# Kernel tuning notes

Measured on AMD Instinct MI355X. Metric: run time of the kernel, lower is better.

## Reference

```python
import jax, jax.numpy as jnp
import numpy as np

B, T, HID = 2, 2048, 3840
H, KV, D = 16, 8, 256
EPS = 1e-6
WINDOW = 1024
THETA_LOCAL = 10000.0
THETA_GLOBAL = 1000000.0


def _rope_tables(theta, t, d):
    inv_freq = 1.0 / (theta ** (jnp.arange(0, d, 2, dtype=jnp.float32) / d))  # (d/2,)
    ang = jnp.arange(t, dtype=jnp.float32)[:, None] * inv_freq[None, :]        # (T, d/2)
    return jnp.cos(ang), jnp.sin(ang)


def setup_inputs() -> dict:
    key = jax.random.key(0)
    ks = jax.random.split(key, 8)
    x = jax.random.normal(ks[0], (B, T, HID), dtype=jnp.float32)
    wq = jax.random.normal(ks[1], (H * D, HID), dtype=jnp.float32) * 0.02
    wk = jax.random.normal(ks[2], (KV * D, HID), dtype=jnp.float32) * 0.02
    wv = jax.random.normal(ks[3], (KV * D, HID), dtype=jnp.float32) * 0.02
    wo = jax.random.normal(ks[4], (HID, H * D), dtype=jnp.float32) * 0.02
    q_norm_w = 1.0 + jax.random.normal(ks[5], (D,), dtype=jnp.float32) * 0.02
    k_norm_w = 1.0 + jax.random.normal(ks[6], (D,), dtype=jnp.float32) * 0.02
    cos_g, sin_g = _rope_tables(THETA_GLOBAL, T, D)
    cos_l, sin_l = _rope_tables(THETA_LOCAL, T, D)
    # causal + sliding-window(1024) additive float mask, shape (1,1,T,T)
    i = jnp.arange(T)[:, None]
    j = jnp.arange(T)[None, :]
    allowed = (j <= i) & (i - j < WINDOW)
    attention_mask = jnp.where(allowed, 0.0, -1e9).astype(jnp.float32)[None, None]
    return {"x": x, "cos_global": cos_g, "sin_global": sin_g, "cos_local": cos_l,
            "sin_local": sin_l, "attention_mask": attention_mask,
            "wq": wq, "wk": wk, "wv": wv, "wo": wo,
            "q_norm_w": q_norm_w, "k_norm_w": k_norm_w}


def _rms_norm(x, w):
    # add=False variant: x * rsqrt(mean(x^2)+eps) * w, computed in fp32
    norm = jax.lax.rsqrt(jnp.mean(jnp.square(x), axis=-1, keepdims=True) + EPS)
    return x * norm * w


def _apply_rope(x, cos, sin):
    # x: (B, H, T, D); cos/sin: (T, D/2)
    t = x.shape[2]
    c = cos[:t][None, None]
    s = sin[:t][None, None]
    x1, x2 = x[..., : x.shape[-1] // 2], x[..., x.shape[-1] // 2 :]
    return jnp.concatenate([x1 * c - x2 * s, x2 * c + x1 * s], axis=-1)


def reference(x, cos_global, sin_global, cos_local, sin_local, attention_mask,
              wq, wk, wv, wo, q_norm_w, k_norm_w):
    b, t, _ = x.shape
    q = (x @ wq.T).reshape(b, t, H, D).transpose(0, 2, 1, 3)   # (B,H,T,D)
    k = (x @ wk.T).reshape(b, t, KV, D).transpose(0, 2, 1, 3)  # (B,KV,T,D)
    v = (x @ wv.T).reshape(b, t, KV, D).transpose(0, 2, 1, 3)
    q = _rms_norm(q, q_norm_w)
    k = _rms_norm(k, k_norm_w)
    # layer_idx=0 -> sliding-window layer -> local rope
    q = _apply_rope(q, cos_local, sin_local)
    k = _apply_rope(k, cos_local, sin_local)
    rep = H // KV
    k = jnp.repeat(k, rep, axis=1)  # repeat_interleave over head dim
    v = jnp.repeat(v, rep, axis=1)
    scale = 1.0 / jnp.sqrt(jnp.float32(D))
    scores = jnp.einsum("bhqd,bhkd->bhqk", q, k) * scale + attention_mask
    attn = jax.nn.softmax(scores, axis=-1)
    out = jnp.einsum("bhqk,bhkd->bhqd", attn, v)
    out = out.transpose(0, 2, 1, 3).reshape(b, t, H * D)
    return out @ wo.T
```

## Files before the change

### kernel.cpp

```cpp
#include <hip/hip_runtime.h>
#include <hip/hip_bf16.h>

typedef __hip_bfloat16 BF;
typedef __attribute__((ext_vector_type(8))) short short8;
typedef __attribute__((ext_vector_type(4))) float f32x4;

#define DEV __device__ __forceinline__

DEV void gll16(const BF* g, BF* l) {
  __builtin_amdgcn_global_load_lds(
      (const __attribute__((address_space(1))) void*)g,
      (__attribute__((address_space(3))) void*)l, 16, 0, 0);
}

DEV unsigned short bfbits(float f) {
  BF b = __float2bfloat16(f);
  return *reinterpret_cast<unsigned short*>(&b);
}

DEV ushort4 cvt4(const float4 v) {
  return make_ushort4(bfbits(v.x), bfbits(v.y), bfbits(v.z), bfbits(v.w));
}

__global__ void cvt_fused(const float* __restrict__ x, const float* __restrict__ wq,
                          const float* __restrict__ wk, const float* __restrict__ wv,
                          BF* __restrict__ Xbf, BF* __restrict__ Wqkv) {
  const int stride = gridDim.x * blockDim.x;
  for (int i = blockIdx.x * blockDim.x + threadIdx.x; i < 11796480; i += stride) {
    const float* src;
    ushort4* dst;
    int off;
    if (i < 3932160)      { src = x;  off = i;           dst = (ushort4*)Xbf; }
    else if (i < 7864320) { src = wq; off = i - 3932160; dst = (ushort4*)Wqkv; }
    else if (i < 9830400) { src = wk; off = i - 7864320; dst = (ushort4*)(Wqkv + 4096 * 3840); }
    else                  { src = wv; off = i - 9830400; dst = (ushort4*)(Wqkv + 6144 * 3840); }
    dst[off] = cvt4(((const float4*)src)[off]);
  }
}

__global__ void f32_to_bf16_pad_k(const float* __restrict__ in, BF* __restrict__ out, int n4) {
  int i = blockIdx.x * blockDim.x + threadIdx.x;
  if (i >= n4) return;
  const int r = i >> 10;
  const int c = i & 1023;
  ((ushort4*)out)[r * 1040 + c] = cvt4(((const float4*)in)[i]);
}

#define PHASE(MH, KK, READB, STAGE, TAIL)                                            \
  {                                                                                  \
    short8 af[4];                                                                    \
    const BF* Ap = Ax + (KK)*8192;                                                   \
    _Pragma("unroll") for (int m = 0; m < 4; ++m)                                    \
        af[m] = *(const short8*)&Ap[(wm*128 + (MH)*64 + m*16 + l15) * 32 + rd8];     \
    if (READB) {                                                                     \
      const BF* Bp = Bx + (KK)*8192;                                                 \
      _Pragma("unroll") for (int n = 0; n < 4; ++n)                                  \
          breg[n] = *(const short8*)&Bp[(wn*64 + n*16 + l15) * 32 + rd8];            \
    }                                                                                \
    STAGE                                                                            \
    __builtin_amdgcn_s_barrier();                                                    \
    asm volatile("s_waitcnt lgkmcnt(0)" ::: "memory");                               \
    __builtin_amdgcn_sched_barrier(0);                                               \
    __builtin_amdgcn_s_setprio(1);                                                   \
    _Pragma("unroll") for (int m = 0; m < 4; ++m)                                    \
      _Pragma("unroll") for (int n = 0; n < 4; ++n)                                  \
        acc[(MH)*4 + m][n] =                                                         \
            __builtin_amdgcn_mfma_f32_16x16x32_bf16(af[m], breg[n], acc[(MH)*4+m][n], 0, 0, 0); \
    __builtin_amdgcn_s_setprio(0);                                                   \
    TAIL                                                                             \
    __builtin_amdgcn_s_barrier();                                                    \
  }

#define STG2(SRC, RST, DST) { gll16((SRC), (DST)); gll16((SRC) + (RST), (DST) + 4096); }

template <typename CT>
DEV void gemm256_body(const BF* __restrict__ A, const BF* __restrict__ Bm,
                      CT* __restrict__ C, const int M, const int N, const int K,
                      const int lda, const int ldb) {
  extern __shared__ __align__(16) BF lds[];
  BF* ldsA = lds;
  BF* ldsB = lds + 32768;
  const int ntl = N >> 8;
  const int mtl = M >> 8;
  int mt, nt;
  if (mtl == 16 && ntl == 32) {
    const int x = blockIdx.x & 7;
    const int c = blockIdx.x >> 3;
    mt = ((x >> 2) << 3) + (c >> 3);
    nt = ((x & 3) << 3) + (c & 7);
  } else {
    const int cpx = gridDim.x >> 3;
    const int swzb = (blockIdx.x & 7) * cpx + (blockIdx.x >> 3);
    mt = swzb / ntl;
    nt = swzb % ntl;
  }
  const int m0 = mt << 8, n0 = nt << 8;
  const int tid = threadIdx.x, lane = tid & 63, w = tid >> 6;
  const int l15 = lane & 15, g = lane >> 4;
  const int wm = w >> 2, wn = w & 3;
  const int rd8 = (g ^ ((l15 >> 1) & 3)) << 3;
  const int trow = tid >> 2;
  const int scol = ((lane & 3) ^ ((lane >> 3) & 3)) << 3;
  const BF* aS = A + (size_t)(m0 + trow) * lda + scol;
  const BF* bS = Bm + (size_t)(n0 + trow) * ldb + scol;
  const size_t rstpA = (size_t)128 * lda;
  const size_t rstpB = (size_t)128 * ldb;
  BF* dA = ldsA + w * 512;
  BF* dB = ldsB + w * 512;
  const int NT = K >> 6;

  f32x4 acc[8][4];
#pragma unroll
  for (int m = 0; m < 8; ++m)
#pragma unroll
    for (int n = 0; n < 4; ++n) acc[m][n] = (f32x4){0.f, 0.f, 0.f, 0.f};
  short8 breg[4];

  STG2(aS, rstpA, dA);
  STG2(bS, rstpB, dB);
  STG2(aS + 32, rstpA, dA + 8192);
  STG2(bS + 32, rstpB, dB + 8192);
  STG2(aS + 64, rstpA, dA + 16384);
  STG2(bS + 64, rstpB, dB + 16384);
  asm volatile("s_waitcnt vmcnt(8)" ::: "memory");
  __builtin_amdgcn_sched_barrier(0);
  __builtin_amdgcn_s_barrier();

  for (int t = 0; t < NT; ++t) {
    const int bX = (t & 1) << 14;
    const int bY = bX ^ 16384;
    const BF* Ax = ldsA + bX;
    const BF* Bx = ldsB + bX;
    const int kc1 = (t + 1) << 6, kc2 = (t + 2) << 6;
    const bool s1 = (t + 1 < NT), s2 = (t + 2 < NT);
    PHASE(0, 0, 1, if (s1) STG2(aS + kc1 + 32, rstpA, dA + bY + 8192);, )
    PHASE(1, 0, 0, if (s1) STG2(bS + kc1 + 32, rstpB, dB + bY + 8192);,
          { asm volatile("s_waitcnt vmcnt(8)" ::: "memory");
            __builtin_amdgcn_sched_barrier(0); } )
    PHASE(0, 1, 1, if (s2) STG2(aS + kc2, rstpA, dA + bX);, )
    PHASE(1, 1, 0, if (s2) STG2(bS + kc2, rstpB, dB + bX);,
          if (s2) { asm volatile("s_waitcnt vmcnt(8)" ::: "memory");
                    __builtin_amdgcn_sched_barrier(0); }
          else    { asm volatile("s_waitcnt vmcnt(0)" ::: "memory");
                    __builtin_amdgcn_sched_barrier(0); } )
  }

#pragma unroll
  for (int mi = 0; mi < 8; ++mi) {
    const int gr = m0 + wm * 128 + mi * 16 + g * 4;
#pragma unroll
    for (int n = 0; n < 4; ++n) {
      const int gc = n0 + wn * 64 + n * 16 + l15;
#pragma unroll
      for (int r = 0; r < 4; ++r) {
        const float v = acc[mi][n][r];
        if constexpr (sizeof(CT) == 2)
          C[(size_t)(gr + r) * N + gc] = __float2bfloat16(v);
        else
          C[(size_t)(gr + r) * N + gc] = v;
      }
    }
  }
}

__global__ __launch_bounds__(512, 2) void gemm_qkv(const BF* __restrict__ A,
                                                   const BF* __restrict__ Bm,
                                                   BF* __restrict__ C,
                                                   int M, int N, int K, int lda, int ldb) {
  gemm256_body<BF>(A, Bm, C, M, N, K, lda, ldb);
}
__global__ __launch_bounds__(512, 2) void gemm_out(const BF* __restrict__ A,
                                                   const BF* __restrict__ Bm,
                                                   float* __restrict__ C,
                                                   int M, int N, int K, int lda, int ldb) {
  gemm256_body<float>(A, Bm, C, M, N, K, lda, ldb);
}

__global__ __launch_bounds__(256) void rmsrope(const BF* __restrict__ C1,
                                               BF* __restrict__ Qo, BF* __restrict__ Ko,
                                               const float* __restrict__ cosl,
                                               const float* __restrict__ sinl,
                                               const float* __restrict__ qw,
                                               const float* __restrict__ kw) {
  const int gwid = (blockIdx.x * 256 + threadIdx.x) >> 6;
  const int lane = threadIdx.x & 63;
  const int slot = gwid % 24;
  const int bt = gwid / 24;
  const int b = bt >> 11, t = bt & 2047;
  const BF* src;
  BF* dst;
  const float* wgt;
  if (slot < 16) {
    src = C1 + (size_t)bt * 8192 + slot * 256;
    dst = Qo + ((size_t)(b * 16 + slot) * 2048 + t) * 256;
    wgt = qw;
  } else {
    const int kv = slot - 16;
    src = C1 + (size_t)bt * 8192 + 4096 + kv * 256;
    dst = Ko + ((size_t)(b * 8 + kv) * 2048 + t) * 256;
    wgt = kw;
  }
  const int d2 = lane * 2;
  const ushort2 lo = *(const ushort2*)((const unsigned short*)src + d2);
  const ushort2 hi = *(const ushort2*)((const unsigned short*)src + 128 + d2);
  float x0 = __bfloat162float(*(const BF*)&lo.x);
  float x1 = __bfloat162float(*(const BF*)&lo.y);
  float x2 = __bfloat162float(*(const BF*)&hi.x);
  float x3 = __bfloat162float(*(const BF*)&hi.y);
  float ss = x0 * x0 + x1 * x1 + x2 * x2 + x3 * x3;
#pragma unroll
  for (int mm = 32; mm >= 1; mm >>= 1) ss += __shfl_xor(ss, mm);
  const float nrm = rsqrtf(ss * (1.f / 256.f) + 1e-6f);
  const float2 wlo = *(const float2*)(wgt + d2);
  const float2 whi = *(const float2*)(wgt + 128 + d2);
  x0 *= nrm * wlo.x;
  x1 *= nrm * wlo.y;
  x2 *= nrm * whi.x;
  x3 *= nrm * whi.y;
  const float2 c = *(const float2*)(cosl + t * 128 + d2);
  const float2 s = *(const float2*)(sinl + t * 128 + d2);
  ushort2 olo, ohi;
  olo.x = bfbits(x0 * c.x - x2 * s.x);
  olo.y = bfbits(x1 * c.y - x3 * s.y);
  ohi.x = bfbits(x2 * c.x + x0 * s.x);
  ohi.y = bfbits(x3 * c.y + x1 * s.y);
  *(ushort2*)((unsigned short*)dst + d2) = olo;
  *(ushort2*)((unsigned short*)dst + 128 + d2) = ohi;
}

__global__ void vtrans(const BF* __restrict__ C1, BF* __restrict__ Vt) {
  __shared__ BF tile[32][33];
  const int bz = blockIdx.z;
  const int tt = blockIdx.x;
  const int dt = blockIdx.y;
  const int x = threadIdx.x, y0 = threadIdx.y;
  const int b = bz >> 3, kv = bz & 7;
#pragma unroll
  for (int yy = y0; yy < 32; yy += 8) {
    const int t = tt * 32 + yy, d = dt * 32 + x;
    tile[yy][x] = C1[((size_t)(b * 2048 + t)) * 8192 + 6144 + kv * 256 + d];
  }
  __syncthreads();
#pragma unroll
  for (int yy = y0; yy < 32; yy += 8) {
    const int d = dt * 32 + yy, t = tt * 32 + x;
    Vt[((size_t)bz * 256 + d) * 2048 + t] = tile[x][yy];
  }
}

__global__ __launch_bounds__(512, 1) void attn_fwd(const BF* __restrict__ Q,
                                                   const BF* __restrict__ K,
                                                   const BF* __restrict__ Vt,
                                                   BF* __restrict__ O) {
  __shared__ __align__(16) BF Ks[64 * 256];
  __shared__ __align__(16) BF Vs[256 * 64];
  __shared__ __align__(16) BF Ps[8][1024];
  const int tid = threadIdx.x;
  const int lane = tid & 63;
  const int w = tid >> 6;
  const int wh = w >> 2;
  const int wq = w & 3;
  const int l15 = lane & 15;
  const int g = lane >> 4;
  const int qt = blockIdx.x;
  const int bp = blockIdx.y;
  const int b = bp >> 3, kvh = bp & 7;
  const int h = kvh * 2 + wh;
  const int q0 = qt << 6;
  const BF* Qb = Q + ((size_t)(b * 16 + h) * 2048 + q0) * 256;
  const BF* Kb = K + (size_t)(b * 8 + kvh) * 2048 * 256;
  const BF* Vb = Vt + (size_t)(b * 8 + kvh) * 256 * 2048;

  short8 qf[8];
  {
    const BF* qr = Qb + (wq * 16 + l15) * 256 + g * 8;
#pragma unroll
    for (int kk = 0; kk < 8; ++kk) qf[kk] = *(const short8*)(qr + kk * 32);
  }
  f32x4 oacc[16];
#pragma unroll
  for (int i = 0; i < 16; ++i) oacc[i] = (f32x4){0.f, 0.f, 0.f, 0.f};
  float m_r[4] = {-1e30f, -1e30f, -1e30f, -1e30f};
  float l_r[4] = {0.f, 0.f, 0.f, 0.f};

  const int kt_lo = (q0 > 1023) ? ((q0 - 1023) >> 6) : 0;
  for (int kt = kt_lo; kt <= qt; ++kt) {
    const int tk = kt << 6;
#pragma unroll
    for (int i = 0; i < 4; ++i) {
      const int li = w * 4 + i;
      {
        const int row = li * 2 + (lane >> 5);
        const int ch = lane & 31;
        gll16(Kb + (size_t)(tk + row) * 256 + ((ch ^ (row & 7)) << 3), Ks + li * 512);
      }
      {
        const int row = li * 8 + (lane >> 3);
        const int ch = lane & 7;
        gll16(Vb + (size_t)row * 2048 + tk + ((ch ^ (row & 7)) << 3), Vs + li * 512);
      }
    }
    __syncthreads();

    f32x4 sa[4];
#pragma unroll
    for (int i2 = 0; i2 < 4; ++i2) sa[i2] = (f32x4){0.f, 0.f, 0.f, 0.f};
#pragma unroll
    for (int kk = 0; kk < 8; ++kk) {
      const int d = kk * 32 + g * 8;
#pragma unroll
      for (int blk = 0; blk < 4; ++blk) {
        const int row = blk * 16 + l15;
        const short8 kf = *(const short8*)&Ks[row * 256 + (d ^ ((row & 7) << 3))];
        sa[blk] = __builtin_amdgcn_mfma_f32_16x16x32_bf16(qf[kk], kf, sa[blk], 0, 0, 0);
      }
    }

    float al4[4];
#pragma unroll
    for (int r = 0; r < 4; ++r) {
      const int qi = q0 + wq * 16 + g * 4 + r;
      float pv[4];
      float tmax = -1e30f;
#pragma unroll
      for (int blk = 0; blk < 4; ++blk) {
        const int ki = tk + blk * 16 + l15;
        float sv = sa[blk][r] * 0.0625f;
        const bool ok = (ki <= qi) && (qi - ki < 1024);
        sv = ok ? sv : -1e30f;
        pv[blk] = sv;
        tmax = fmaxf(tmax, sv);
      }
#pragma unroll
      for (int mm = 1; mm < 16; mm <<= 1) tmax = fmaxf(tmax, __shfl_xor(tmax, mm));
      const float mn = fmaxf(m_r[r], tmax);
      const float alpha = __expf(m_r[r] - mn);
      float tsum = 0.f;
#pragma unroll
      for (int blk = 0; blk < 4; ++blk) {
        const float p = __expf(pv[blk] - mn);
        pv[blk] = p;
        tsum += p;
      }
#pragma unroll
      for (int mm = 1; mm < 16; mm <<= 1) tsum += __shfl_xor(tsum, mm);
      l_r[r] = l_r[r] * alpha + tsum;
      m_r[r] = mn;
      al4[r] = alpha;
      const int prow = g * 4 + r;
#pragma unroll
      for (int blk = 0; blk < 4; ++blk) {
        const int col = blk * 16 + l15;
        Ps[w][prow * 64 + (col ^ ((prow & 7) << 3))] = __float2bfloat16(pv[blk]);
      }
    }
#pragma unroll
    for (int db = 0; db < 16; ++db)
#pragma unroll
      for (int r = 0; r < 4; ++r) oacc[db][r] *= al4[r];

#pragma unroll
    for (int kk2 = 0; kk2 < 2; ++kk2) {
      const int k8 = kk2 * 32 + g * 8;
      const short8 pf = *(const short8*)&Ps[w][l15 * 64 + (k8 ^ ((l15 & 7) << 3))];
#pragma unroll
      for (int db = 0; db < 16; ++db) {
        const int vrow = db * 16 + l15;
        const short8 vf = *(const short8*)&Vs[vrow * 64 + (k8 ^ ((vrow & 7) << 3))];
        oacc[db] = __builtin_amdgcn_mfma_f32_16x16x32_bf16(pf, vf, oacc[db], 0, 0, 0);
      }
    }
    __syncthreads();
  }

#pragma unroll
  for (int r = 0; r < 4; ++r) l_r[r] = 1.f / l_r[r];
  const size_t orow0 = (size_t)(b * 2048 + q0 + wq * 16 + g * 4);
#pragma unroll
  for (int r = 0; r < 4; ++r) {
    BF* op = O + (orow0 + r) * 4160 + h * 256 + l15;
#pragma unroll
    for (int db = 0; db < 16; ++db) op[db * 16] = __float2bfloat16(oacc[db][r] * l_r[r]);
  }
}

extern "C" void kernel_launch(void* const* d_in, const int* in_sizes, int n_in,
                              void* d_out, int out_size, void* d_ws, size_t ws_size,
                              hipStream_t stream) {
  (void)in_sizes; (void)n_in; (void)out_size;
  const float* x    = (const float*)d_in[0];
  const float* cosl = (const float*)d_in[3];
  const float* sinl = (const float*)d_in[4];
  const float* wq   = (const float*)d_in[6];
  const float* wk   = (const float*)d_in[7];
  const float* wv   = (const float*)d_in[8];
  const float* wo   = (const float*)d_in[9];
  const float* qw   = (const float*)d_in[10];
  const float* kw   = (const float*)d_in[11];
  float* out = (float*)d_out;
  char* ws = (char*)d_ws;
  if (ws_size < 161480704ull) return;

  BF* Wqkv = (BF*)(ws + 0);
  BF* Xbf  = (BF*)(ws + 62914560);
  BF* C1   = (BF*)(ws + 94371840);
  BF* Qb   = (BF*)(ws + 0);
  BF* Kb   = (BF*)(ws + 33554432);
  BF* Vt   = (BF*)(ws + 62914560);
  BF* AO   = (BF*)(ws + 94371840);
  BF* Wo   = (BF*)(ws + 128450560);

  hipFuncSetAttribute(reinterpret_cast<const void*>(gemm_qkv),
                      hipFuncAttributeMaxDynamicSharedMemorySize, 131072);
  hipFuncSetAttribute(reinterpret_cast<const void*>(gemm_out),
                      hipFuncAttributeMaxDynamicSharedMemorySize, 131072);

  cvt_fused<<<2048, 256, 0, stream>>>(x, wq, wk, wv, Xbf, Wqkv);

  gemm_qkv<<<512, 512, 131072, stream>>>(Xbf, Wqkv, C1, 4096, 8192, 3840, 3840, 3840);
  rmsrope<<<24576, 256, 0, stream>>>(C1, Qb, Kb, cosl, sinl, qw, kw);
  vtrans<<<dim3(64, 8, 16), dim3(32, 8), 0, stream>>>(C1, Vt);
  {
    const int n4 = (3840 * 4096) >> 2;
    f32_to_bf16_pad_k<<<(n4 + 255) / 256, 256, 0, stream>>>(wo, Wo, n4);
  }
  attn_fwd<<<dim3(32, 16), 512, 0, stream>>>(Qb, Kb, Vt, AO);
  gemm_out<<<240, 512, 131072, stream>>>(AO, Wo, out, 4096, 3840, 4096, 4160, 4160);
}
```

Before: 567.5 us.

## Double attention query tile, vectorize V transpose, fold Wo conversion into cvt kernel

The attention kernel now handles 128 query rows per block (two 64-row groups per wave), so each K/V tile staged in LDS is reused twice and the K/V load traffic is halved. The cost is double the accumulator registers and a grid of only 256 blocks, which can underfill the GPU and add wasted masked tiles near the diagonal. The V transpose is rewritten with 64x64 tiles and 4-wide vector loads and stores. The Wo fp32-to-bf16 conversion is merged into the fused convert kernel, removing one launch; this needs a larger workspace so Wo no longer overlaps other buffers.

```diff
diff --git a/kernel.cpp b/kernel.cpp
--- a/kernel.cpp
+++ b/kernel.cpp
@@ -24,26 +24,25 @@
 
 __global__ void cvt_fused(const float* __restrict__ x, const float* __restrict__ wq,
                           const float* __restrict__ wk, const float* __restrict__ wv,
-                          BF* __restrict__ Xbf, BF* __restrict__ Wqkv) {
+                          const float* __restrict__ wo,
+                          BF* __restrict__ Xbf, BF* __restrict__ Wqkv, BF* __restrict__ Wo) {
   const int stride = gridDim.x * blockDim.x;
-  for (int i = blockIdx.x * blockDim.x + threadIdx.x; i < 11796480; i += stride) {
-    const float* src;
-    ushort4* dst;
-    int off;
-    if (i < 3932160)      { src = x;  off = i;           dst = (ushort4*)Xbf; }
-    else if (i < 7864320) { src = wq; off = i - 3932160; dst = (ushort4*)Wqkv; }
-    else if (i < 9830400) { src = wk; off = i - 7864320; dst = (ushort4*)(Wqkv + 4096 * 3840); }
-    else                  { src = wv; off = i - 9830400; dst = (ushort4*)(Wqkv + 6144 * 3840); }
-    dst[off] = cvt4(((const float4*)src)[off]);
-  }
-}
-
-__global__ void f32_to_bf16_pad_k(const float* __restrict__ in, BF* __restrict__ out, int n4) {
-  int i = blockIdx.x * blockDim.x + threadIdx.x;
-  if (i >= n4) return;
-  const int r = i >> 10;
-  const int c = i & 1023;
-  ((ushort4*)out)[r * 1040 + c] = cvt4(((const float4*)in)[i]);
+  for (int i = blockIdx.x * blockDim.x + threadIdx.x; i < 15728640; i += stride) {
+    if (i < 11796480) {
+      const float* src;
+      ushort4* dst;
+      int off;
+      if (i < 3932160)      { src = x;  off = i;           dst = (ushort4*)Xbf; }
+      else if (i < 7864320) { src = wq; off = i - 3932160; dst = (ushort4*)Wqkv; }
+      else if (i < 9830400) { src = wk; off = i - 7864320; dst = (ushort4*)(Wqkv + 4096 * 3840); }
+      else                  { src = wv; off = i - 9830400; dst = (ushort4*)(Wqkv + 6144 * 3840); }
+      dst[off] = cvt4(((const float4*)src)[off]);
+    } else {
+      const int off = i - 11796480;
+      const int r = off >> 10, c = off & 1023;
+      ((ushort4*)Wo)[r * 1040 + c] = cvt4(((const float4*)wo)[off]);
+    }
+  }
 }
 
 #define PHASE(MH, KK, READB, STAGE, TAIL)                                            \
@@ -228,23 +227,35 @@
   *(ushort2*)((unsigned short*)dst + 128 + d2) = ohi;
 }
 
-__global__ void vtrans(const BF* __restrict__ C1, BF* __restrict__ Vt) {
-  __shared__ BF tile[32][33];
+__global__ __launch_bounds__(256) void vtrans(const BF* __restrict__ C1, BF* __restrict__ Vt) {
+  __shared__ BF tile[64][68];
   const int bz = blockIdx.z;
   const int tt = blockIdx.x;
   const int dt = blockIdx.y;
-  const int x = threadIdx.x, y0 = threadIdx.y;
+  const int tid = threadIdx.x;
+  const int r16 = tid >> 4;
+  const int c16 = tid & 15;
   const int b = bz >> 3, kv = bz & 7;
 #pragma unroll
-  for (int yy = y0; yy < 32; yy += 8) {
-    const int t = tt * 32 + yy, d = dt * 32 + x;
-    tile[yy][x] = C1[((size_t)(b * 2048 + t)) * 8192 + 6144 + kv * 256 + d];
+  for (int p = 0; p < 4; ++p) {
+    const int tr = p * 16 + r16;
+    const int t = tt * 64 + tr;
+    const int d = dt * 64 + c16 * 4;
+    *(ushort4*)&tile[tr][c16 * 4] =
+        *(const ushort4*)&C1[((size_t)(b * 2048 + t)) * 8192 + 6144 + kv * 256 + d];
   }
   __syncthreads();
 #pragma unroll
-  for (int yy = y0; yy < 32; yy += 8) {
-    const int d = dt * 32 + yy, t = tt * 32 + x;
-    Vt[((size_t)bz * 256 + d) * 2048 + t] = tile[x][yy];
+  for (int p = 0; p < 4; ++p) {
+    const int dr = p * 16 + r16;
+    const int d = dt * 64 + dr;
+    const int t4 = c16 * 4;
+    ushort4 o;
+    o.x = *(const unsigned short*)&tile[t4 + 0][dr];
+    o.y = *(const unsigned short*)&tile[t4 + 1][dr];
+    o.z = *(const unsigned short*)&tile[t4 + 2][dr];
+    o.w = *(const unsigned short*)&tile[t4 + 3][dr];
+    *(ushort4*)&Vt[((size_t)bz * 256 + d) * 2048 + tt * 64 + t4] = o;
   }
 }
 
@@ -254,7 +265,7 @@
                                                    BF* __restrict__ O) {
   __shared__ __align__(16) BF Ks[64 * 256];
   __shared__ __align__(16) BF Vs[256 * 64];
-  __shared__ __align__(16) BF Ps[8][1024];
+  __shared__ __align__(16) BF Ps[8][2048];
   const int tid = threadIdx.x;
   const int lane = tid & 63;
   const int w = tid >> 6;
@@ -266,25 +277,32 @@
   const int bp = blockIdx.y;
   const int b = bp >> 3, kvh = bp & 7;
   const int h = kvh * 2 + wh;
-  const int q0 = qt << 6;
+  const int q0 = qt << 7;
   const BF* Qb = Q + ((size_t)(b * 16 + h) * 2048 + q0) * 256;
   const BF* Kb = K + (size_t)(b * 8 + kvh) * 2048 * 256;
   const BF* Vb = Vt + (size_t)(b * 8 + kvh) * 256 * 2048;
 
-  short8 qf[8];
-  {
-    const BF* qr = Qb + (wq * 16 + l15) * 256 + g * 8;
-#pragma unroll
-    for (int kk = 0; kk < 8; ++kk) qf[kk] = *(const short8*)(qr + kk * 32);
-  }
-  f32x4 oacc[16];
-#pragma unroll
-  for (int i = 0; i < 16; ++i) oacc[i] = (f32x4){0.f, 0.f, 0.f, 0.f};
-  float m_r[4] = {-1e30f, -1e30f, -1e30f, -1e30f};
-  float l_r[4] = {0.f, 0.f, 0.f, 0.f};
+  short8 qf[2][8];
+#pragma unroll
+  for (int rg = 0; rg < 2; ++rg) {
+    const BF* qr = Qb + (rg * 64 + wq * 16 + l15) * 256 + g * 8;
+#pragma unroll
+    for (int kk = 0; kk < 8; ++kk) qf[rg][kk] = *(const short8*)(qr + kk * 32);
+  }
+  f32x4 oacc[2][16];
+#pragma unroll
+  for (int rg = 0; rg < 2; ++rg)
+#pragma unroll
+    for (int i = 0; i < 16; ++i) oacc[rg][i] = (f32x4){0.f, 0.f, 0.f, 0.f};
+  float m_r[2][4], l_r[2][4];
+#pragma unroll
+  for (int rg = 0; rg < 2; ++rg)
+#pragma unroll
+    for (int r = 0; r < 4; ++r) { m_r[rg][r] = -1e30f; l_r[rg][r] = 0.f; }
 
   const int kt_lo = (q0 > 1023) ? ((q0 - 1023) >> 6) : 0;
-  for (int kt = kt_lo; kt <= qt; ++kt) {
+  const int kt_hi = (q0 + 127) >> 6;
+  for (int kt = kt_lo; kt <= kt_hi; ++kt) {
     const int tk = kt << 6;
 #pragma unroll
     for (int i = 0; i < 4; ++i) {
@@ -302,85 +320,92 @@
     }
     __syncthreads();
 
-    f32x4 sa[4];
-#pragma unroll
-    for (int i2 = 0; i2 < 4; ++i2) sa[i2] = (f32x4){0.f, 0.f, 0.f, 0.f};
-#pragma unroll
-    for (int kk = 0; kk < 8; ++kk) {
-      const int d = kk * 32 + g * 8;
-#pragma unroll
-      for (int blk = 0; blk < 4; ++blk) {
-        const int row = blk * 16 + l15;
-        const short8 kf = *(const short8*)&Ks[row * 256 + (d ^ ((row & 7) << 3))];
-        sa[blk] = __builtin_amdgcn_mfma_f32_16x16x32_bf16(qf[kk], kf, sa[blk], 0, 0, 0);
-      }
-    }
-
-    float al4[4];
+    float al4[2][4];
+#pragma unroll
+    for (int rg = 0; rg < 2; ++rg) {
+      f32x4 sa[4];
+#pragma unroll
+      for (int i2 = 0; i2 < 4; ++i2) sa[i2] = (f32x4){0.f, 0.f, 0.f, 0.f};
+#pragma unroll
+      for (int kk = 0; kk < 8; ++kk) {
+        const int d = kk * 32 + g * 8;
+#pragma unroll
+        for (int blk = 0; blk < 4; ++blk) {
+          const int row = blk * 16 + l15;
+          const short8 kf = *(const short8*)&Ks[row * 256 + (d ^ ((row & 7) << 3))];
+          sa[blk] = __builtin_amdgcn_mfma_f32_16x16x32_bf16(qf[rg][kk], kf, sa[blk], 0, 0, 0);
+        }
+      }
+#pragma unroll
+      for (int r = 0; r < 4; ++r) {
+        const int qi = q0 + rg * 64 + wq * 16 + g * 4 + r;
+        float pv[4];
+        float tmax = -1e30f;
+#pragma unroll
+        for (int blk = 0; blk < 4; ++blk) {
+          const int ki = tk + blk * 16 + l15;
+          float sv = sa[blk][r] * 0.0625f;
+          const bool ok = (ki <= qi) && (qi - ki < 1024);
+          sv = ok ? sv : -1e30f;
+          pv[blk] = sv;
+          tmax = fmaxf(tmax, sv);
+        }
+#pragma unroll
+        for (int mm = 1; mm < 16; mm <<= 1) tmax = fmaxf(tmax, __shfl_xor(tmax, mm));
+        const float mn = fmaxf(m_r[rg][r], tmax);
+        const float alpha = __expf(m_r[rg][r] - mn);
+        float tsum = 0.f;
+#pragma unroll
+        for (int blk = 0; blk < 4; ++blk) {
+          const float p = __expf(pv[blk] - mn);
+          pv[blk] = p;
+          tsum += p;
+        }
+#pragma unroll
+        for (int mm = 1; mm < 16; mm <<= 1) tsum += __shfl_xor(tsum, mm);
+        l_r[rg][r] = l_r[rg][r] * alpha + tsum;
+        m_r[rg][r] = mn;
+        al4[rg][r] = alpha;
+        const int prow = g * 4 + r;
+#pragma unroll
+        for (int blk = 0; blk < 4; ++blk) {
+          const int col = blk * 16 + l15;
+          Ps[w][rg * 1024 + prow * 64 + (col ^ ((prow & 7) << 3))] = __float2bfloat16(pv[blk]);
+        }
+      }
+#pragma unroll
+      for (int db = 0; db < 16; ++db)
+#pragma unroll
+        for (int r = 0; r < 4; ++r) oacc[rg][db][r] *= al4[rg][r];
+    }
+
+#pragma unroll
+    for (int rg = 0; rg < 2; ++rg) {
+#pragma unroll
+      for (int kk2 = 0; kk2 < 2; ++kk2) {
+        const int k8 = kk2 * 32 + g * 8;
+        const short8 pf = *(const short8*)&Ps[w][rg * 1024 + l15 * 64 + (k8 ^ ((l15 & 7) << 3))];
+#pragma unroll
+        for (int db = 0; db < 16; ++db) {
+          const int vrow = db * 16 + l15;
+          const short8 vf = *(const short8*)&Vs[vrow * 64 + (k8 ^ ((vrow & 7) << 3))];
+          oacc[rg][db] = __builtin_amdgcn_mfma_f32_16x16x32_bf16(pf, vf, oacc[rg][db], 0, 0, 0);
+        }
+      }
+    }
+    __syncthreads();
+  }
+
+#pragma unroll
+  for (int rg = 0; rg < 2; ++rg) {
 #pragma unroll
     for (int r = 0; r < 4; ++r) {
-      const int qi = q0 + wq * 16 + g * 4 + r;
-      float pv[4];
-      float tmax = -1e30f;
-#pragma unroll
-      for (int blk = 0; blk < 4; ++blk) {
-        const int ki = tk + blk * 16 + l15;
-        float sv = sa[blk][r] * 0.0625f;
-        const bool ok = (ki <= qi) && (qi - ki < 1024);
-        sv = ok ? sv : -1e30f;
-        pv[blk] = sv;
-        tmax = fmaxf(tmax, sv);
-      }
-#pragma unroll
-      for (int mm = 1; mm < 16; mm <<= 1) tmax = fmaxf(tmax, __shfl_xor(tmax, mm));
-      const float mn = fmaxf(m_r[r], tmax);
-      const float alpha = __expf(m_r[r] - mn);
-      float tsum = 0.f;
-#pragma unroll
-      for (int blk = 0; blk < 4; ++blk) {
-        const float p = __expf(pv[blk] - mn);
-        pv[blk] = p;
-        tsum += p;
-      }
-#pragma unroll
-      for (int mm = 1; mm < 16; mm <<= 1) tsum += __shfl_xor(tsum, mm);
-      l_r[r] = l_r[r] * alpha + tsum;
-      m_r[r] = mn;
-      al4[r] = alpha;
-      const int prow = g * 4 + r;
-#pragma unroll
-      for (int blk = 0; blk < 4; ++blk) {
-        const int col = blk * 16 + l15;
-        Ps[w][prow * 64 + (col ^ ((prow & 7) << 3))] = __float2bfloat16(pv[blk]);
-      }
-    }
-#pragma unroll
-    for (int db = 0; db < 16; ++db)
-#pragma unroll
-      for (int r = 0; r < 4; ++r) oacc[db][r] *= al4[r];
-
-#pragma unroll
-    for (int kk2 = 0; kk2 < 2; ++kk2) {
-      const int k8 = kk2 * 32 + g * 8;
-      const short8 pf = *(const short8*)&Ps[w][l15 * 64 + (k8 ^ ((l15 & 7) << 3))];
-#pragma unroll
-      for (int db = 0; db < 16; ++db) {
-        const int vrow = db * 16 + l15;
-        const short8 vf = *(const short8*)&Vs[vrow * 64 + (k8 ^ ((vrow & 7) << 3))];
-        oacc[db] = __builtin_amdgcn_mfma_f32_16x16x32_bf16(pf, vf, oacc[db], 0, 0, 0);
-      }
-    }
-    __syncthreads();
-  }
-
-#pragma unroll
-  for (int r = 0; r < 4; ++r) l_r[r] = 1.f / l_r[r];
-  const size_t orow0 = (size_t)(b * 2048 + q0 + wq * 16 + g * 4);
-#pragma unroll
-  for (int r = 0; r < 4; ++r) {
-    BF* op = O + (orow0 + r) * 4160 + h * 256 + l15;
-#pragma unroll
-    for (int db = 0; db < 16; ++db) op[db * 16] = __float2bfloat16(oacc[db][r] * l_r[r]);
+      const float li = 1.f / l_r[rg][r];
+      const size_t orow = (size_t)(b * 2048 + q0 + rg * 64 + wq * 16 + g * 4 + r);
+      BF* op = O + orow * 4160 + h * 256 + l15;
+#pragma unroll
+      for (int db = 0; db < 16; ++db) op[db * 16] = __float2bfloat16(oacc[rg][db][r] * li);
+    }
   }
 }
 
@@ -399,7 +424,7 @@
   const float* kw   = (const float*)d_in[11];
   float* out = (float*)d_out;
   char* ws = (char*)d_ws;
-  if (ws_size < 161480704ull) return;
+  if (ws_size < 193429504ull) return;
 
   BF* Wqkv = (BF*)(ws + 0);
   BF* Xbf  = (BF*)(ws + 62914560);
@@ -408,22 +433,18 @@
   BF* Kb   = (BF*)(ws + 33554432);
   BF* Vt   = (BF*)(ws + 62914560);
   BF* AO   = (BF*)(ws + 94371840);
-  BF* Wo   = (BF*)(ws + 128450560);
+  BF* Wo   = (BF*)(ws + 161480704);
 
   hipFuncSetAttribute(reinterpret_cast<const void*>(gemm_qkv),
                       hipFuncAttributeMaxDynamicSharedMemorySize, 131072);
   hipFuncSetAttribute(reinterpret_cast<const void*>(gemm_out),
                       hipFuncAttributeMaxDynamicSharedMemorySize, 131072);
 
-  cvt_fused<<<2048, 256, 0, stream>>>(x, wq, wk, wv, Xbf, Wqkv);
+  cvt_fused<<<2048, 256, 0, stream>>>(x, wq, wk, wv, wo, Xbf, Wqkv, Wo);
 
   gemm_qkv<<<512, 512, 131072, stream>>>(Xbf, Wqkv, C1, 4096, 8192, 3840, 3840, 3840);
   rmsrope<<<24576, 256, 0, stream>>>(C1, Qb, Kb, cosl, sinl, qw, kw);
-  vtrans<<<dim3(64, 8, 16), dim3(32, 8), 0, stream>>>(C1, Vt);
-  {
-    const int n4 = (3840 * 4096) >> 2;
-    f32_to_bf16_pad_k<<<(n4 + 255) / 256, 256, 0, stream>>>(wo, Wo, n4);
-  }
-  attn_fwd<<<dim3(32, 16), 512, 0, stream>>>(Qb, Kb, Vt, AO);
+  vtrans<<<dim3(32, 4, 16), 256, 0, stream>>>(C1, Vt);
+  attn_fwd<<<dim3(16, 16), 512, 0, stream>>>(Qb, Kb, Vt, AO);
   gemm_out<<<240, 512, 131072, stream>>>(AO, Wo, out, 4096, 3840, 4096, 4160, 4160);
 }
```

Measured after the change: 761.4 us. 34.2% more time.
